# Kernel optimization log

Hardware: AMD Instinct MI355X
Metric: run time of the kernel (lower is better)

Reference implementation:

```python
import jax, jax.numpy as jnp
import numpy as np

N_NODES = 100000
N_EDGES = 1600000
NUM_FEATURES = 512
NHID = 256
CHEB_K = 6


def setup_inputs() -> dict:
    key = jax.random.key(0)
    ks = jax.random.split(key, 12)
    x = jax.random.normal(ks[0], (N_NODES, NUM_FEATURES), dtype=jnp.float32)
    edge_index = jax.random.randint(ks[1], (2, N_EDGES), 0, N_NODES, dtype=jnp.int64)
    edge_weight = jax.random.uniform(ks[2], (N_EDGES,), dtype=jnp.float32)
    s = 1.0 / np.sqrt(NUM_FEATURES)
    W1 = jax.random.uniform(ks[3], (NUM_FEATURES, NHID), jnp.float32, -s, s)
    b1 = jnp.zeros((NHID,), jnp.float32)
    s2 = 1.0 / np.sqrt(NHID)
    Wc = jax.random.uniform(ks[4], (CHEB_K, NHID, NHID // 2), jnp.float32, -s2, s2)
    bc = jnp.zeros((NHID // 2,), jnp.float32)
    s3 = 1.0 / np.sqrt(NHID // 2)
    W_out = jax.random.uniform(ks[5], (NHID // 2, 1), jnp.float32, -s3, s3)
    W_root = jax.random.uniform(ks[6], (NHID // 2, 1), jnp.float32, -s3, s3)
    b3 = jnp.zeros((1,), jnp.float32)
    return {"x": x, "edge_index": edge_index, "edge_weight": edge_weight,
            "W1": W1, "b1": b1, "Wc": Wc, "bc": bc,
            "W_out": W_out, "W_root": W_root, "b3": b3}


def _safe_rsqrt(d):
    return jnp.where(d > 0, jax.lax.rsqrt(jnp.where(d > 0, d, 1.0)), 0.0)


def _gcn_conv(x, src, dst, ew, W, b, n):
    # GCNConv: add self-loops (weight 1), sym-normalize, then aggregate x @ W.
    loop = jnp.arange(n)
    src2 = jnp.concatenate([src, loop])
    dst2 = jnp.concatenate([dst, loop])
    ew2 = jnp.concatenate([ew, jnp.ones((n,), ew.dtype)])
    deg = jax.ops.segment_sum(ew2, dst2, num_segments=n)
    dis = _safe_rsqrt(deg)
    norm = dis[src2] * ew2 * dis[dst2]                     # [E+N]
    h = x @ W                                              # [N, out]
    out = jax.ops.segment_sum(h[src2] * norm[:, None], dst2, num_segments=n)
    return out + b


def _cheb_conv(x, src, dst, ew, Wc, bc, n):
    # ChebConv (sym norm, lambda_max=2): L_hat = -D^{-1/2} A D^{-1/2} (diag 0).
    deg = jax.ops.segment_sum(ew, dst, num_segments=n)
    dis = _safe_rsqrt(deg)
    wn = -(dis[src] * ew * dis[dst])                        # [E]

    def lmv(h):  # L_hat @ h
        return jax.ops.segment_sum(h[src] * wn[:, None], dst, num_segments=n)

    Tx0 = x
    out = Tx0 @ Wc[0]
    Tx1 = lmv(x)
    out = out + Tx1 @ Wc[1]
    for k in range(2, Wc.shape[0]):
        Tx2 = 2.0 * lmv(Tx1) - Tx0
        out = out + Tx2 @ Wc[k]
        Tx0, Tx1 = Tx1, Tx2
    return out + bc


def _cluster_gcn_conv(x, src, dst, W_out, W_root, b, n):
    # ClusterGCNConv (diag_lambda=0): out = (D^{-1}(A+I) x) W_out + b + x W_root.
    loop = jnp.arange(n)
    src2 = jnp.concatenate([src, loop])
    dst2 = jnp.concatenate([dst, loop])
    deg = jax.ops.segment_sum(jnp.ones_like(dst2, dtype=x.dtype), dst2, num_segments=n)
    w = (1.0 / jnp.maximum(deg, 1.0))[dst2]                 # [E+N]
    agg = jax.ops.segment_sum(x[src2] * w[:, None], dst2, num_segments=n)
    return agg @ W_out + b + x @ W_root


def reference(x, edge_index, edge_weight, W1, b1, Wc, bc, W_out, W_root, b3):
    n = x.shape[0]
    src, dst = edge_index[0], edge_index[1]
    h = _gcn_conv(x, src, dst, edge_weight, W1, b1, n)
    h = jax.nn.relu(h)
    # dropout is identity in eval mode
    h = _cheb_conv(h, src, dst, edge_weight, Wc, bc, n)
    h = jax.nn.relu(h)
    features = h
    out = _cluster_gcn_conv(h, src, dst, W_out, W_root, b3, n)
    return (out.reshape(-1), features)
```

## Files before the change

kernel.cpp:

```cpp
#include <hip/hip_runtime.h>
#include <cstdint>
#include <cstddef>

typedef __attribute__((ext_vector_type(8))) short bf16x8;
typedef __attribute__((ext_vector_type(4))) float f32x4;

static inline int ceil_div(int a, int b){ return (a + b - 1) / b; }

struct HL { short h, l; };
__device__ inline HL split2(float a){
  unsigned u = __float_as_uint(a);
  unsigned hb = (u + 0x8000u) & 0xFFFF0000u;
  float r = a - __uint_as_float(hb);
  HL o;
  o.h = (short)(hb >> 16);
  o.l = (short)((__float_as_uint(r) + 0x8000u) >> 16);
  return o;
}

__device__ inline unsigned short f2b(float f){
  unsigned u = __float_as_uint(f);
  unsigned r = u + 0x7FFFu + ((u >> 16) & 1u);
  return (unsigned short)(r >> 16);
}
__device__ inline float b2f(unsigned short s){
  return __uint_as_float((unsigned)s << 16);
}

__global__ __launch_bounds__(256) void k_detect(const int* __restrict__ ei32, int E, int* __restrict__ flag){
  int t = blockIdx.x * 256 + threadIdx.x;
  if (t < 4096) {
    long long idx = 2LL * t + 1;
    if (idx < 2LL * E && ei32[idx] != 0) atomicOr(flag, 1);
  }
}

__global__ __launch_bounds__(256) void k_count(const void* __restrict__ ei, int E,
                                               const int* __restrict__ flag, int* __restrict__ cnt){
  int e = blockIdx.x * 256 + threadIdx.x;
  if (e >= E) return;
  int dst = (*flag) ? ((const int*)ei)[(size_t)E + e]
                    : (int)((const long long*)ei)[(size_t)E + e];
  atomicAdd(&cnt[dst], 1);
}

__global__ __launch_bounds__(256) void k_scan_part(const int* __restrict__ cnt, int* __restrict__ bsum, int N){
  int base = blockIdx.x * 1024 + threadIdx.x * 4;
  int s = 0;
  if (base + 4 <= N){
    int4 v = *(const int4*)(cnt + base);
    s = v.x + v.y + v.z + v.w;
  } else {
    for (int i = base; i < N; ++i) s += cnt[i];
  }
#pragma unroll
  for (int off = 32; off; off >>= 1) s += __shfl_xor(s, off);
  __shared__ int ws[4];
  if ((threadIdx.x & 63) == 0) ws[threadIdx.x >> 6] = s;
  __syncthreads();
  if (threadIdx.x == 0) bsum[blockIdx.x] = ws[0] + ws[1] + ws[2] + ws[3];
}

__global__ __launch_bounds__(1024) void k_scan_bsum(int* __restrict__ bsum, int nb){
  __shared__ int sh[1024];
  int t = threadIdx.x;
  int v = (t < nb) ? bsum[t] : 0;
  sh[t] = v; __syncthreads();
  for (int off = 1; off < 1024; off <<= 1){
    int u = (t >= off) ? sh[t - off] : 0;
    __syncthreads();
    sh[t] += u;
    __syncthreads();
  }
  if (t < nb) bsum[t] = sh[t] - v;
}

__global__ __launch_bounds__(256) void k_scan_write(const int* __restrict__ cnt, const int* __restrict__ bsum,
                                                    int* __restrict__ row_ptr, int* __restrict__ cursor,
                                                    int N, int E){
  int t = threadIdx.x;
  int base = blockIdx.x * 1024 + t * 4;
  int v0 = 0, v1 = 0, v2 = 0, v3 = 0;
  if (base + 4 <= N){
    int4 v = *(const int4*)(cnt + base);
    v0 = v.x; v1 = v.y; v2 = v.z; v3 = v.w;
  } else {
    if (base + 0 < N) v0 = cnt[base + 0];
    if (base + 1 < N) v1 = cnt[base + 1];
    if (base + 2 < N) v2 = cnt[base + 2];
    if (base + 3 < N) v3 = cnt[base + 3];
  }
  int s = v0 + v1 + v2 + v3;
  int lane = t & 63;
  int inc = s;
#pragma unroll
  for (int off = 1; off < 64; off <<= 1){
    int u = __shfl_up(inc, off);
    if (lane >= off) inc += u;
  }
  __shared__ int ws[4];
  if (lane == 63) ws[t >> 6] = inc;
  __syncthreads();
  int wid = t >> 6;
  int woff = 0;
  for (int i = 0; i < wid; ++i) woff += ws[i];
  int exc = bsum[blockIdx.x] + woff + inc - s;
  int p0 = exc, p1 = p0 + v0, p2 = p1 + v1, p3 = p2 + v2;
  if (base + 0 < N){ row_ptr[base + 0] = p0; cursor[base + 0] = p0; }
  if (base + 1 < N){ row_ptr[base + 1] = p1; cursor[base + 1] = p1; }
  if (base + 2 < N){ row_ptr[base + 2] = p2; cursor[base + 2] = p2; }
  if (base + 3 < N){ row_ptr[base + 3] = p3; cursor[base + 3] = p3; }
  if (blockIdx.x == 0 && t == 0) row_ptr[N] = E;
}

__global__ __launch_bounds__(256) void k_fill(const void* __restrict__ ei, const float* __restrict__ ew, int E,
                                              const int* __restrict__ flag, int* __restrict__ cursor,
                                              uint2* __restrict__ csr_sw){
  int e = blockIdx.x * 256 + threadIdx.x;
  if (e >= E) return;
  int src, dst;
  if (*flag){ src = ((const int*)ei)[e]; dst = ((const int*)ei)[(size_t)E + e]; }
  else      { src = (int)((const long long*)ei)[e]; dst = (int)((const long long*)ei)[(size_t)E + e]; }
  int pos = atomicAdd(&cursor[dst], 1);
  csr_sw[pos] = make_uint2((unsigned)src, __float_as_uint(ew[e]));
}

__global__ __launch_bounds__(256) void k_degrees(const int* __restrict__ row_ptr, const uint2* __restrict__ csr_sw,
                                                 float* __restrict__ dis1, float* __restrict__ dis2,
                                                 float* __restrict__ invw, int N){
  int r = blockIdx.x * 256 + threadIdx.x;
  if (r >= N) return;
  int e0 = row_ptr[r], e1 = row_ptr[r + 1];
  float s = 0.f;
  for (int e = e0; e < e1; ++e) s += __uint_as_float(csr_sw[e].y);
  dis1[r] = rsqrtf(s + 1.0f);
  dis2[r] = (s > 0.0f) ? rsqrtf(s) : 0.0f;
  invw[r] = 1.0f / (float)(e1 - e0 + 1);
}

__global__ __launch_bounds__(256) void k_norm(const uint2* __restrict__ csr_sw,
                                              const float* __restrict__ dis1, const float* __restrict__ dis2,
                                              uint2* __restrict__ pk_gcn, uint2* __restrict__ pk_cheb, int E){
  int e = blockIdx.x * 256 + threadIdx.x;
  if (e >= E) return;
  uint2 p = csr_sw[e];
  int s = (int)p.x;
  float w = __uint_as_float(p.y);
  pk_gcn[e]  = make_uint2(p.x, __float_as_uint(w * dis1[s]));
  pk_cheb[e] = make_uint2(p.x, __float_as_uint(w * dis2[s]));
}

__global__ __launch_bounds__(256) void k_prep_w(const float* __restrict__ W, short* __restrict__ Wh,
                                                short* __restrict__ Wl, int K, int N){
  int idx = blockIdx.x * 256 + threadIdx.x;
  if (idx >= K * N) return;
  int n = idx / K, k = idx - n * K;
  HL s = split2(W[(size_t)k * N + n]);
  Wh[idx] = s.h; Wl[idx] = s.l;
}

__global__ __launch_bounds__(256) void k_prep_wc(const float* __restrict__ Wc, short* __restrict__ Wh){
  int idx = blockIdx.x * 256 + threadIdx.x;
  if (idx >= 768 * 256) return;
  int n = idx >> 8, k = idx & 255;
  Wh[idx] = (short)f2b(Wc[(size_t)(n >> 7) * 256 * 128 + (size_t)k * 128 + (n & 127)]);
}

__global__ __launch_bounds__(256) void k_gemm_mfma(
    const float* __restrict__ A,
    const short* __restrict__ Bh, const short* __restrict__ Bl,
    unsigned short* __restrict__ Cb,
    int M, int Ncols, int K, int nbm)
{
  __shared__ short Ah[128][40];
  __shared__ short Bhs[128][40];
  __shared__ short Bls[128][40];
  int bid = blockIdx.x;
  int g = bid & 7, j = bid >> 3;
  int m_tile = g + 8 * (j >> 1);
  int n_tile = j & 1;
  if (m_tile >= nbm) return;
  int m0 = m_tile * 128, n0 = n_tile * 128;
  int t = threadIdx.x;
  int lane = t & 63, wid = t >> 6;
  int wr = wid >> 1, wc = wid & 1;
  int fr = lane & 15, fq = lane >> 4;
  int srow = t >> 1, skh = (t & 1) << 4;

  f32x4 acc[4][4];
#pragma unroll
  for (int i = 0; i < 4; ++i)
#pragma unroll
    for (int jj = 0; jj < 4; ++jj) acc[i][jj] = (f32x4){0.f, 0.f, 0.f, 0.f};

  bool aval = (m0 + srow) < M;
  const float* Aptr = A + (size_t)(m0 + srow) * K + skh;
  const short* Bhp = Bh + (size_t)(n0 + srow) * K + skh;
  const short* Blp = Bl + (size_t)(n0 + srow) * K + skh;

  float4 a0, a1, a2, a3;
  if (aval){
    const float4* ap = (const float4*)Aptr;
    a0 = ap[0]; a1 = ap[1]; a2 = ap[2]; a3 = ap[3];
  } else a0 = a1 = a2 = a3 = make_float4(0.f, 0.f, 0.f, 0.f);

  for (int k0 = 0; k0 < K; k0 += 32){
    bf16x8 h0, h1;
    h0[0]=(short)f2b(a0.x); h0[1]=(short)f2b(a0.y); h0[2]=(short)f2b(a0.z); h0[3]=(short)f2b(a0.w);
    h0[4]=(short)f2b(a1.x); h0[5]=(short)f2b(a1.y); h0[6]=(short)f2b(a1.z); h0[7]=(short)f2b(a1.w);
    h1[0]=(short)f2b(a2.x); h1[1]=(short)f2b(a2.y); h1[2]=(short)f2b(a2.z); h1[3]=(short)f2b(a2.w);
    h1[4]=(short)f2b(a3.x); h1[5]=(short)f2b(a3.y); h1[6]=(short)f2b(a3.z); h1[7]=(short)f2b(a3.w);
    *(bf16x8*)&Ah[srow][skh]     = h0;
    *(bf16x8*)&Ah[srow][skh + 8] = h1;
    {
      const bf16x8* bp = (const bf16x8*)(Bhp + k0);
      *(bf16x8*)&Bhs[srow][skh]     = bp[0];
      *(bf16x8*)&Bhs[srow][skh + 8] = bp[1];
      const bf16x8* cp = (const bf16x8*)(Blp + k0);
      *(bf16x8*)&Bls[srow][skh]     = cp[0];
      *(bf16x8*)&Bls[srow][skh + 8] = cp[1];
    }
    __syncthreads();
    bool more = (k0 + 32) < K;
    float4 n0v, n1v, n2v, n3v;
    if (more && aval){
      const float4* ap = (const float4*)(Aptr + k0 + 32);
      n0v = ap[0]; n1v = ap[1]; n2v = ap[2]; n3v = ap[3];
    } else n0v = n1v = n2v = n3v = make_float4(0.f, 0.f, 0.f, 0.f);
    bf16x8 afh[4], bfh[4], bfl[4];
#pragma unroll
    for (int m = 0; m < 4; ++m){
      int r = wr * 64 + m * 16 + fr;
      afh[m] = *(const bf16x8*)&Ah[r][fq * 8];
    }
#pragma unroll
    for (int n = 0; n < 4; ++n){
      int r = wc * 64 + n * 16 + fr;
      bfh[n] = *(const bf16x8*)&Bhs[r][fq * 8];
      bfl[n] = *(const bf16x8*)&Bls[r][fq * 8];
    }
#pragma unroll
    for (int m = 0; m < 4; ++m)
#pragma unroll
      for (int n = 0; n < 4; ++n){
        acc[m][n] = __builtin_amdgcn_mfma_f32_16x16x32_bf16(afh[m], bfh[n], acc[m][n], 0, 0, 0);
        acc[m][n] = __builtin_amdgcn_mfma_f32_16x16x32_bf16(afh[m], bfl[n], acc[m][n], 0, 0, 0);
      }
    __syncthreads();
    a0 = n0v; a1 = n1v; a2 = n2v; a3 = n3v;
  }
#pragma unroll
  for (int m = 0; m < 4; ++m){
#pragma unroll
    for (int n = 0; n < 4; ++n){
      int col = n0 + wc * 64 + n * 16 + fr;
#pragma unroll
      for (int r = 0; r < 4; ++r){
        int row = m0 + wr * 64 + m * 16 + fq * 4 + r;
        if (row < M){
          Cb[(size_t)row * Ncols + col] = f2b(acc[m][n][r]);
        }
      }
    }
  }
}

__global__ __launch_bounds__(256) void k_gemm_mfma2(
    const unsigned short* __restrict__ Ahg,
    const short* __restrict__ Bh,
    unsigned short* __restrict__ Cb, unsigned short* __restrict__ C5c,
    int M, int Ncols, int K, int nbm)
{
  __shared__ short Ah[128][40];
  __shared__ short Bhs[128][40];
  int bid = blockIdx.x;
  int g = bid & 7, j = bid >> 3;
  int m_tile = g + 8 * (j / 6);
  int n_tile = j - 6 * (j / 6);
  if (m_tile >= nbm) return;
  int m0 = m_tile * 128, n0 = n_tile * 128;
  int t = threadIdx.x;
  int lane = t & 63, wid = t >> 6;
  int wr = wid >> 1, wc = wid & 1;
  int fr = lane & 15, fq = lane >> 4;
  int srow = t >> 1, skh = (t & 1) << 4;

  f32x4 acc[4][4];
#pragma unroll
  for (int i = 0; i < 4; ++i)
#pragma unroll
    for (int jj = 0; jj < 4; ++jj) acc[i][jj] = (f32x4){0.f, 0.f, 0.f, 0.f};

  bool aval = (m0 + srow) < M;
  const unsigned short* Ahp = Ahg + (size_t)(m0 + srow) * K + skh;
  const short* Bhp = Bh + (size_t)(n0 + srow) * K + skh;

  bf16x8 ch0, ch1;
  if (aval){
    const bf16x8* ah = (const bf16x8*)Ahp;
    ch0 = ah[0]; ch1 = ah[1];
  } else {
    bf16x8 z = (bf16x8){0,0,0,0,0,0,0,0};
    ch0 = ch1 = z;
  }

  for (int k0 = 0; k0 < K; k0 += 32){
    *(bf16x8*)&Ah[srow][skh]     = ch0;
    *(bf16x8*)&Ah[srow][skh + 8] = ch1;
    {
      const bf16x8* bp = (const bf16x8*)(Bhp + k0);
      *(bf16x8*)&Bhs[srow][skh]     = bp[0];
      *(bf16x8*)&Bhs[srow][skh + 8] = bp[1];
    }
    __syncthreads();
    bool more = (k0 + 32) < K;
    bf16x8 nh0, nh1;
    if (more && aval){
      const bf16x8* ah = (const bf16x8*)(Ahp + k0 + 32);
      nh0 = ah[0]; nh1 = ah[1];
    } else {
      bf16x8 z = (bf16x8){0,0,0,0,0,0,0,0};
      nh0 = nh1 = z;
    }
    bf16x8 afh[4], bfh[4];
#pragma unroll
    for (int m = 0; m < 4; ++m){
      int r = wr * 64 + m * 16 + fr;
      afh[m] = *(const bf16x8*)&Ah[r][fq * 8];
    }
#pragma unroll
    for (int n = 0; n < 4; ++n){
      int r = wc * 64 + n * 16 + fr;
      bfh[n] = *(const bf16x8*)&Bhs[r][fq * 8];
    }
#pragma unroll
    for (int m = 0; m < 4; ++m)
#pragma unroll
      for (int n = 0; n < 4; ++n){
        acc[m][n] = __builtin_amdgcn_mfma_f32_16x16x32_bf16(afh[m], bfh[n], acc[m][n], 0, 0, 0);
      }
    __syncthreads();
    ch0 = nh0; ch1 = nh1;
  }
#pragma unroll
  for (int m = 0; m < 4; ++m){
#pragma unroll
    for (int n = 0; n < 4; ++n){
      int col = n0 + wc * 64 + n * 16 + fr;
#pragma unroll
      for (int r = 0; r < 4; ++r){
        int row = m0 + wr * 64 + m * 16 + fq * 4 + r;
        if (row < M){
          unsigned short v = f2b(acc[m][n][r]);
          Cb[(size_t)row * Ncols + col] = v;
          if (n_tile == 5) C5c[(size_t)row * 128 + (col - 640)] = v;
        }
      }
    }
  }
}

__global__ __launch_bounds__(256) void k_gcn_agg(
    const unsigned short* __restrict__ h0b,
    const uint2* __restrict__ pk, const int* __restrict__ row_ptr,
    const float* __restrict__ dis1, const float* __restrict__ b1,
    unsigned short* __restrict__ h1b, int N){
  int lane = threadIdx.x & 63;
  int r = blockIdx.x * 4 + (threadIdx.x >> 6);
  if (r >= N) return;
  float dr = dis1[r];
  ushort4 sv = ((const ushort4*)(h0b + (size_t)r * 256))[lane];
  float4 inner = make_float4(b2f(sv.x) * dr, b2f(sv.y) * dr, b2f(sv.z) * dr, b2f(sv.w) * dr);
  int e0 = row_ptr[r], e1 = row_ptr[r + 1];
  int e = e0;
  for (; e + 8 <= e1; e += 8){
    uint2 pv[8]; ushort4 vi[8];
#pragma unroll
    for (int q = 0; q < 8; ++q) pv[q] = pk[e + q];
#pragma unroll
    for (int q = 0; q < 8; ++q) vi[q] = ((const ushort4*)(h0b + (size_t)pv[q].x * 256))[lane];
#pragma unroll
    for (int q = 0; q < 8; ++q){
      float w = __uint_as_float(pv[q].y);
      inner.x = fmaf(w, b2f(vi[q].x), inner.x);
      inner.y = fmaf(w, b2f(vi[q].y), inner.y);
      inner.z = fmaf(w, b2f(vi[q].z), inner.z);
      inner.w = fmaf(w, b2f(vi[q].w), inner.w);
    }
  }
  for (; e < e1; ++e){
    uint2 p = pk[e];
    float w = __uint_as_float(p.y);
    ushort4 v = ((const ushort4*)(h0b + (size_t)p.x * 256))[lane];
    inner.x = fmaf(w, b2f(v.x), inner.x); inner.y = fmaf(w, b2f(v.y), inner.y);
    inner.z = fmaf(w, b2f(v.z), inner.z); inner.w = fmaf(w, b2f(v.w), inner.w);
  }
  float4 bb = ((const float4*)b1)[lane];
  ushort4 o;
  o.x = f2b(fmaxf(fmaf(inner.x, dr, bb.x), 0.f));
  o.y = f2b(fmaxf(fmaf(inner.y, dr, bb.y), 0.f));
  o.z = f2b(fmaxf(fmaf(inner.z, dr, bb.z), 0.f));
  o.w = f2b(fmaxf(fmaf(inner.w, dr, bb.w), 0.f));
  ((ushort4*)(h1b + (size_t)r * 256))[lane] = o;
}

__global__ __launch_bounds__(256) void k_cheb_spmm2(
    const unsigned short* __restrict__ Ck, int ckstride,
    const unsigned short* __restrict__ sub16, int substride,
    const float* __restrict__ subf,
    const unsigned short* __restrict__ srcb, int sstride,
    float* __restrict__ dst, unsigned short* __restrict__ dstb,
    const uint2* __restrict__ pk, const int* __restrict__ row_ptr,
    const float* __restrict__ dis2, float coef, int N){
  int lane = threadIdx.x & 63;
  int r = blockIdx.x * 4 + (threadIdx.x >> 6);
  if (r >= N) return;
  float2 inner = make_float2(0.f, 0.f);
  int e0 = row_ptr[r], e1 = row_ptr[r + 1];
  int e = e0;
  for (; e + 8 <= e1; e += 8){
    uint2 pv[8]; unsigned vi[8];
#pragma unroll
    for (int q = 0; q < 8; ++q) pv[q] = pk[e + q];
#pragma unroll
    for (int q = 0; q < 8; ++q) vi[q] = ((const unsigned*)(srcb + (size_t)pv[q].x * sstride))[lane];
#pragma unroll
    for (int q = 0; q < 8; ++q){
      float w = __uint_as_float(pv[q].y);
      inner.x = fmaf(w, __uint_as_float(vi[q] << 16), inner.x);
      inner.y = fmaf(w, __uint_as_float(vi[q] & 0xFFFF0000u), inner.y);
    }
  }
  for (; e < e1; ++e){
    uint2 p = pk[e];
    float w = __uint_as_float(p.y);
    unsigned v = ((const unsigned*)(srcb + (size_t)p.x * sstride))[lane];
    inner.x = fmaf(w, __uint_as_float(v << 16), inner.x);
    inner.y = fmaf(w, __uint_as_float(v & 0xFFFF0000u), inner.y);
  }
  float c = coef * dis2[r];
  unsigned ckv = ((const unsigned*)(Ck + (size_t)r * ckstride))[lane];
  float rx = fmaf(c, inner.x, __uint_as_float(ckv << 16));
  float ry = fmaf(c, inner.y, __uint_as_float(ckv & 0xFFFF0000u));
  if (sub16){
    unsigned sv = ((const unsigned*)(sub16 + (size_t)r * substride))[lane];
    rx -= __uint_as_float(sv << 16);
    ry -= __uint_as_float(sv & 0xFFFF0000u);
  }
  if (subf){
    float2 s2 = ((const float2*)(subf + (size_t)r * 128))[lane];
    rx -= s2.x;
    ry -= s2.y;
  }
  ((float2*)(dst + (size_t)r * 128))[lane] = make_float2(rx, ry);
  if (dstb){
    unsigned pkd = (unsigned)f2b(rx) | ((unsigned)f2b(ry) << 16);
    ((unsigned*)(dstb + (size_t)r * 128))[lane] = pkd;
  }
}

__global__ __launch_bounds__(256) void k_spmm_final(
    const unsigned short* __restrict__ Ck, int ckstride,
    const float* __restrict__ subf,
    const unsigned short* __restrict__ srcb, int sstride,
    const float* __restrict__ bc, const float* __restrict__ W_out, const float* __restrict__ W_root,
    float* __restrict__ feat, float* __restrict__ p, float* __restrict__ wr,
    const uint2* __restrict__ pk, const int* __restrict__ row_ptr,
    const float* __restrict__ dis2, float coef, int N){
  int lane = threadIdx.x & 63;
  int r = blockIdx.x * 4 + (threadIdx.x >> 6);
  if (r >= N) return;
  float2 inner = make_float2(0.f, 0.f);
  int e0 = row_ptr[r], e1 = row_ptr[r + 1];
  int e = e0;
  for (; e + 8 <= e1; e += 8){
    uint2 pv[8]; unsigned vi[8];
#pragma unroll
    for (int q = 0; q < 8; ++q) pv[q] = pk[e + q];
#pragma unroll
    for (int q = 0; q < 8; ++q) vi[q] = ((const unsigned*)(srcb + (size_t)pv[q].x * sstride))[lane];
#pragma unroll
    for (int q = 0; q < 8; ++q){
      float w = __uint_as_float(pv[q].y);
      inner.x = fmaf(w, __uint_as_float(vi[q] << 16), inner.x);
      inner.y = fmaf(w, __uint_as_float(vi[q] & 0xFFFF0000u), inner.y);
    }
  }
  for (; e < e1; ++e){
    uint2 pp = pk[e];
    float w = __uint_as_float(pp.y);
    unsigned v = ((const unsigned*)(srcb + (size_t)pp.x * sstride))[lane];
    inner.x = fmaf(w, __uint_as_float(v << 16), inner.x);
    inner.y = fmaf(w, __uint_as_float(v & 0xFFFF0000u), inner.y);
  }
  float c = coef * dis2[r];
  unsigned ckv = ((const unsigned*)(Ck + (size_t)r * ckstride))[lane];
  float rx = fmaf(c, inner.x, __uint_as_float(ckv << 16));
  float ry = fmaf(c, inner.y, __uint_as_float(ckv & 0xFFFF0000u));
  float2 s2 = ((const float2*)(subf + (size_t)r * 128))[lane];
  rx -= s2.x;
  ry -= s2.y;
  float2 bb = ((const float2*)bc)[lane];
  rx = fmaxf(rx + bb.x, 0.f);
  ry = fmaxf(ry + bb.y, 0.f);
  ((float2*)(feat + (size_t)r * 128))[lane] = make_float2(rx, ry);
  float2 wo = ((const float2*)W_out)[lane];
  float2 wrt = ((const float2*)W_root)[lane];
  float pp2 = rx * wo.x + ry * wo.y;
  float rr = rx * wrt.x + ry * wrt.y;
#pragma unroll
  for (int off = 32; off; off >>= 1){
    pp2 += __shfl_xor(pp2, off);
    rr += __shfl_xor(rr, off);
  }
  if (lane == 0){ p[r] = pp2; wr[r] = rr; }
}

__global__ __launch_bounds__(256) void k_out(const float* __restrict__ p, const float* __restrict__ wr,
    const float* __restrict__ invw, const uint2* __restrict__ pk, const int* __restrict__ row_ptr,
    const float* __restrict__ b3, float* __restrict__ out, int N){
  int r = blockIdx.x * 256 + threadIdx.x;
  if (r >= N) return;
  float s = p[r];
  int e0 = row_ptr[r], e1 = row_ptr[r + 1];
  int e = e0;
  float acc[8] = {0.f,0.f,0.f,0.f,0.f,0.f,0.f,0.f};
  for (; e + 8 <= e1; e += 8){
    int si[8];
#pragma unroll
    for (int q = 0; q < 8; ++q) si[q] = (int)pk[e + q].x;
#pragma unroll
    for (int q = 0; q < 8; ++q) acc[q] += p[si[q]];
  }
  for (; e < e1; ++e) acc[0] += p[(int)pk[e].x];
  s += ((acc[0]+acc[1])+(acc[2]+acc[3])) + ((acc[4]+acc[5])+(acc[6]+acc[7]));
  out[r] = invw[r] * s + wr[r] + b3[0];
}

extern "C" void kernel_launch(void* const* d_in, const int* in_sizes, int n_in,
                              void* d_out, int out_size, void* d_ws, size_t ws_size,
                              hipStream_t stream){
  const float* x      = (const float*)d_in[0];
  const void*  ei     = d_in[1];
  const float* ew     = (const float*)d_in[2];
  const float* W1     = (const float*)d_in[3];
  const float* b1     = (const float*)d_in[4];
  const float* Wc     = (const float*)d_in[5];
  const float* bc     = (const float*)d_in[6];
  const float* W_out  = (const float*)d_in[7];
  const float* W_root = (const float*)d_in[8];
  const float* b3     = (const float*)d_in[9];
  const int N = in_sizes[0] / 512;
  const int E = in_sizes[2];

  char* w = (char*)d_ws;
  auto alloc = [&](size_t bytes)->void*{ void* r = (void*)w; w += (bytes + 255) & ~(size_t)255; return r; };
  unsigned short* h1b = (unsigned short*)alloc((size_t)N * 256 * 2 * 2);
  float* B0 = (float*)h1b;
  float* B1 = B0 + (size_t)N * 128;
  float* B2 = (float*)alloc((size_t)N * 128 * 4);
  unsigned short* C5c = (unsigned short*)B2;
  unsigned short* CC  = (unsigned short*)alloc((size_t)N * 768 * 2);
  unsigned short* h0b = (unsigned short*)alloc((size_t)N * 256 * 2);
  unsigned short* Bb0 = h0b;
  unsigned short* Bb1 = h0b + (size_t)N * 128;
  uint2* csr_sw  = (uint2*)alloc((size_t)E * 8);
  uint2* pk_gcn  = (uint2*)alloc((size_t)E * 8);
  uint2* pk_cheb = (uint2*)alloc((size_t)E * 8);
  int*   row_ptr = (int*)  alloc((size_t)(N + 1) * 4);
  int*   cursor  = (int*)  alloc((size_t)N * 4);
  int*   cnt     = (int*)  alloc((size_t)N * 4);
  int*   bsum    = (int*)  alloc((size_t)1024 * 4);
  float* dis1    = (float*)alloc((size_t)N * 4);
  float* dis2    = (float*)alloc((size_t)N * 4);
  float* invw    = (float*)alloc((size_t)N * 4);
  float* pbuf    = (float*)alloc((size_t)N * 4);
  float* wrbuf   = (float*)alloc((size_t)N * 4);
  short* W1t_h   = (short*)alloc((size_t)512 * 256 * 2);
  short* W1t_l   = (short*)alloc((size_t)512 * 256 * 2);
  short* Wct_h   = (short*)alloc((size_t)768 * 256 * 2);
  int*   flag    = (int*)  alloc(256);

  hipMemsetAsync(cnt, 0, (size_t)N * 4, stream);
  hipMemsetAsync(flag, 0, 4, stream);

  k_detect<<<16, 256, 0, stream>>>((const int*)ei, E, flag);
  k_count<<<ceil_div(E, 256), 256, 0, stream>>>(ei, E, flag, cnt);
  int nb = ceil_div(N, 1024);
  k_scan_part<<<nb, 256, 0, stream>>>(cnt, bsum, N);
  k_scan_bsum<<<1, 1024, 0, stream>>>(bsum, nb);
  k_scan_write<<<nb, 256, 0, stream>>>(cnt, bsum, row_ptr, cursor, N, E);
  k_fill<<<ceil_div(E, 256), 256, 0, stream>>>(ei, ew, E, flag, cursor, csr_sw);
  k_degrees<<<ceil_div(N, 256), 256, 0, stream>>>(row_ptr, csr_sw, dis1, dis2, invw, N);
  k_norm<<<ceil_div(E, 256), 256, 0, stream>>>(csr_sw, dis1, dis2, pk_gcn, pk_cheb, E);

  k_prep_w<<<ceil_div(512 * 256, 256), 256, 0, stream>>>(W1, W1t_h, W1t_l, 512, 256);
  k_prep_wc<<<ceil_div(768 * 256, 256), 256, 0, stream>>>(Wc, Wct_h);

  int nbm = ceil_div(N, 128);
  int grid1 = 8 * 2 * ceil_div(nbm, 8);
  k_gemm_mfma<<<grid1, 256, 0, stream>>>(x, W1t_h, W1t_l, h0b, N, 256, 512, nbm);
  k_gcn_agg<<<ceil_div(N, 4), 256, 0, stream>>>(h0b, pk_gcn, row_ptr, dis1, b1, h1b, N);

  int grid2 = 8 * 6 * ceil_div(nbm, 8);
  k_gemm_mfma2<<<grid2, 256, 0, stream>>>(h1b, Wct_h, CC, C5c, N, 768, 256, nbm);

  auto spmm = [&](const unsigned short* Ck, const unsigned short* s16, int s16s, const float* sf,
                  const unsigned short* src, int ss, float* dst, unsigned short* dstb, float coef){
    k_cheb_spmm2<<<ceil_div(N, 4), 256, 0, stream>>>(Ck, 768, s16, s16s, sf, src, ss, dst, dstb,
        pk_cheb, row_ptr, dis2, coef, N);
  };
  spmm(CC + 4*128, nullptr, 0, nullptr, C5c, 128, B0, Bb0, -2.f);
  spmm(CC + 3*128, C5c, 128, nullptr, Bb0, 128, B1, Bb1, -2.f);
  spmm(CC + 2*128, nullptr, 0, B0, Bb1, 128, B2, Bb0, -2.f);
  spmm(CC + 1*128, nullptr, 0, B1, Bb0, 128, B0, Bb1, -2.f);

  float* out  = (float*)d_out;
  float* feat = out + N;
  k_spmm_final<<<ceil_div(N, 4), 256, 0, stream>>>(CC + 0*128, 768, B2, Bb1, 128,
      bc, W_out, W_root, feat, pbuf, wrbuf, pk_cheb, row_ptr, dis2, -1.f, N);
  k_out<<<ceil_div(N, 256), 256, 0, stream>>>(pbuf, wrbuf, invw, pk_cheb, row_ptr, b3, out, N);
}
```

Measured before the change: 1.037 ms.

## Build CSR via two-level bucket partition with shared-memory atomics

```diff
diff --git a/kernel.cpp b/kernel.cpp
--- a/kernel.cpp
+++ b/kernel.cpp
@@ -27,6 +27,8 @@
   return __uint_as_float((unsigned)s << 16);
 }
 
+#define EPB 4096
+
 __global__ __launch_bounds__(256) void k_detect(const int* __restrict__ ei32, int E, int* __restrict__ flag){
   int t = blockIdx.x * 256 + threadIdx.x;
   if (t < 4096) {
@@ -35,107 +37,135 @@
   }
 }
 
-__global__ __launch_bounds__(256) void k_count(const void* __restrict__ ei, int E,
-                                               const int* __restrict__ flag, int* __restrict__ cnt){
-  int e = blockIdx.x * 256 + threadIdx.x;
-  if (e >= E) return;
-  int dst = (*flag) ? ((const int*)ei)[(size_t)E + e]
-                    : (int)((const long long*)ei)[(size_t)E + e];
-  atomicAdd(&cnt[dst], 1);
-}
-
-__global__ __launch_bounds__(256) void k_scan_part(const int* __restrict__ cnt, int* __restrict__ bsum, int N){
-  int base = blockIdx.x * 1024 + threadIdx.x * 4;
-  int s = 0;
-  if (base + 4 <= N){
-    int4 v = *(const int4*)(cnt + base);
-    s = v.x + v.y + v.z + v.w;
-  } else {
-    for (int i = base; i < N; ++i) s += cnt[i];
-  }
-#pragma unroll
-  for (int off = 32; off; off >>= 1) s += __shfl_xor(s, off);
-  __shared__ int ws[4];
-  if ((threadIdx.x & 63) == 0) ws[threadIdx.x >> 6] = s;
+__global__ __launch_bounds__(256) void k_hist(const void* __restrict__ ei, int E,
+                                              const int* __restrict__ flag, int* __restrict__ block_hist){
+  __shared__ int h[512];
+  for (int i = threadIdx.x; i < 512; i += 256) h[i] = 0;
   __syncthreads();
-  if (threadIdx.x == 0) bsum[blockIdx.x] = ws[0] + ws[1] + ws[2] + ws[3];
-}
-
-__global__ __launch_bounds__(1024) void k_scan_bsum(int* __restrict__ bsum, int nb){
-  __shared__ int sh[1024];
+  int base = blockIdx.x * EPB;
+  bool is32 = (*flag != 0);
+  for (int i = 0; i < 16; ++i){
+    int e = base + i * 256 + threadIdx.x;
+    if (e < E){
+      int dst = is32 ? ((const int*)ei)[(size_t)E + e] : (int)((const long long*)ei)[(size_t)E + e];
+      atomicAdd(&h[dst >> 8], 1);
+    }
+  }
+  __syncthreads();
+  for (int i = threadIdx.x; i < 512; i += 256) block_hist[blockIdx.x * 512 + i] = h[i];
+}
+
+__global__ __launch_bounds__(64) void k_colscan(const int* __restrict__ block_hist, int* __restrict__ off_hist,
+                                                int* __restrict__ bucket_total, int nblk){
+  int k = blockIdx.x;
+  int lane = threadIdx.x;
+  int carry = 0;
+  for (int c = 0; c * 64 < nblk; ++c){
+    int b = c * 64 + lane;
+    int v = (b < nblk) ? block_hist[b * 512 + k] : 0;
+    int inc = v;
+#pragma unroll
+    for (int off = 1; off < 64; off <<= 1){
+      int u = __shfl_up(inc, off);
+      if (lane >= off) inc += u;
+    }
+    if (b < nblk) off_hist[b * 512 + k] = carry + inc - v;
+    carry += __shfl(inc, 63);
+  }
+  if (lane == 0) bucket_total[k] = carry;
+}
+
+__global__ __launch_bounds__(512) void k_bucketbase(const int* __restrict__ bucket_total,
+                                                    int* __restrict__ bucket_base,
+                                                    int* __restrict__ row_ptr, int N, int E){
+  __shared__ int sh[512];
   int t = threadIdx.x;
-  int v = (t < nb) ? bsum[t] : 0;
+  int v = bucket_total[t];
   sh[t] = v; __syncthreads();
-  for (int off = 1; off < 1024; off <<= 1){
+  for (int off = 1; off < 512; off <<= 1){
     int u = (t >= off) ? sh[t - off] : 0;
     __syncthreads();
     sh[t] += u;
     __syncthreads();
   }
-  if (t < nb) bsum[t] = sh[t] - v;
-}
-
-__global__ __launch_bounds__(256) void k_scan_write(const int* __restrict__ cnt, const int* __restrict__ bsum,
-                                                    int* __restrict__ row_ptr, int* __restrict__ cursor,
-                                                    int N, int E){
+  bucket_base[t] = sh[t] - v;
+  if (t == 511) bucket_base[512] = sh[511];
+  if (t == 0) row_ptr[N] = E;
+}
+
+__global__ __launch_bounds__(256) void k_partition(const void* __restrict__ ei, const float* __restrict__ ew,
+                                                   int E, const int* __restrict__ flag,
+                                                   const int* __restrict__ off_hist,
+                                                   const int* __restrict__ bucket_base,
+                                                   uint2* __restrict__ part){
+  __shared__ int cur[512];
+  for (int i = threadIdx.x; i < 512; i += 256)
+    cur[i] = off_hist[blockIdx.x * 512 + i] + bucket_base[i];
+  __syncthreads();
+  int base = blockIdx.x * EPB;
+  bool is32 = (*flag != 0);
+  for (int i = 0; i < 16; ++i){
+    int e = base + i * 256 + threadIdx.x;
+    if (e < E){
+      int src, dst;
+      if (is32){ src = ((const int*)ei)[e]; dst = ((const int*)ei)[(size_t)E + e]; }
+      else     { src = (int)((const long long*)ei)[e]; dst = (int)((const long long*)ei)[(size_t)E + e]; }
+      int pos = atomicAdd(&cur[dst >> 8], 1);
+      part[pos] = make_uint2((unsigned)src | ((unsigned)(dst & 255) << 20), __float_as_uint(ew[e]));
+    }
+  }
+}
+
+__global__ __launch_bounds__(256) void k_bucket_csr(const uint2* __restrict__ part,
+                                                    const int* __restrict__ bucket_base,
+                                                    uint2* __restrict__ csr_sw, int* __restrict__ row_ptr,
+                                                    float* __restrict__ dis1, float* __restrict__ dis2,
+                                                    float* __restrict__ invw, int N){
+  __shared__ int cnt[256];
+  __shared__ float wsum[256];
+  __shared__ int cursor[256];
+  __shared__ int ws[4];
+  int k = blockIdx.x;
   int t = threadIdx.x;
-  int base = blockIdx.x * 1024 + t * 4;
-  int v0 = 0, v1 = 0, v2 = 0, v3 = 0;
-  if (base + 4 <= N){
-    int4 v = *(const int4*)(cnt + base);
-    v0 = v.x; v1 = v.y; v2 = v.z; v3 = v.w;
-  } else {
-    if (base + 0 < N) v0 = cnt[base + 0];
-    if (base + 1 < N) v1 = cnt[base + 1];
-    if (base + 2 < N) v2 = cnt[base + 2];
-    if (base + 3 < N) v3 = cnt[base + 3];
-  }
-  int s = v0 + v1 + v2 + v3;
+  int base = bucket_base[k], end = bucket_base[k + 1];
+  cnt[t] = 0; wsum[t] = 0.f;
+  __syncthreads();
+  for (int i = base + t; i < end; i += 256){
+    uint2 rec = part[i];
+    int dstl = (rec.x >> 20) & 255;
+    atomicAdd(&cnt[dstl], 1);
+    atomicAdd(&wsum[dstl], __uint_as_float(rec.y));
+  }
+  __syncthreads();
+  int v = cnt[t];
   int lane = t & 63;
-  int inc = s;
+  int inc = v;
 #pragma unroll
   for (int off = 1; off < 64; off <<= 1){
     int u = __shfl_up(inc, off);
     if (lane >= off) inc += u;
   }
-  __shared__ int ws[4];
   if (lane == 63) ws[t >> 6] = inc;
   __syncthreads();
-  int wid = t >> 6;
   int woff = 0;
-  for (int i = 0; i < wid; ++i) woff += ws[i];
-  int exc = bsum[blockIdx.x] + woff + inc - s;
-  int p0 = exc, p1 = p0 + v0, p2 = p1 + v1, p3 = p2 + v2;
-  if (base + 0 < N){ row_ptr[base + 0] = p0; cursor[base + 0] = p0; }
-  if (base + 1 < N){ row_ptr[base + 1] = p1; cursor[base + 1] = p1; }
-  if (base + 2 < N){ row_ptr[base + 2] = p2; cursor[base + 2] = p2; }
-  if (base + 3 < N){ row_ptr[base + 3] = p3; cursor[base + 3] = p3; }
-  if (blockIdx.x == 0 && t == 0) row_ptr[N] = E;
-}
-
-__global__ __launch_bounds__(256) void k_fill(const void* __restrict__ ei, const float* __restrict__ ew, int E,
-                                              const int* __restrict__ flag, int* __restrict__ cursor,
-                                              uint2* __restrict__ csr_sw){
-  int e = blockIdx.x * 256 + threadIdx.x;
-  if (e >= E) return;
-  int src, dst;
-  if (*flag){ src = ((const int*)ei)[e]; dst = ((const int*)ei)[(size_t)E + e]; }
-  else      { src = (int)((const long long*)ei)[e]; dst = (int)((const long long*)ei)[(size_t)E + e]; }
-  int pos = atomicAdd(&cursor[dst], 1);
-  csr_sw[pos] = make_uint2((unsigned)src, __float_as_uint(ew[e]));
-}
-
-__global__ __launch_bounds__(256) void k_degrees(const int* __restrict__ row_ptr, const uint2* __restrict__ csr_sw,
-                                                 float* __restrict__ dis1, float* __restrict__ dis2,
-                                                 float* __restrict__ invw, int N){
-  int r = blockIdx.x * 256 + threadIdx.x;
-  if (r >= N) return;
-  int e0 = row_ptr[r], e1 = row_ptr[r + 1];
-  float s = 0.f;
-  for (int e = e0; e < e1; ++e) s += __uint_as_float(csr_sw[e].y);
-  dis1[r] = rsqrtf(s + 1.0f);
-  dis2[r] = (s > 0.0f) ? rsqrtf(s) : 0.0f;
-  invw[r] = 1.0f / (float)(e1 - e0 + 1);
+  for (int i = 0; i < (t >> 6); ++i) woff += ws[i];
+  int exc = woff + inc - v;
+  int node = k * 256 + t;
+  if (node < N){
+    row_ptr[node] = base + exc;
+    float s = wsum[t];
+    dis1[node] = rsqrtf(s + 1.0f);
+    dis2[node] = (s > 0.f) ? rsqrtf(s) : 0.f;
+    invw[node] = 1.0f / (float)(v + 1);
+  }
+  cursor[t] = exc;
+  __syncthreads();
+  for (int i = base + t; i < end; i += 256){
+    uint2 rec = part[i];
+    int dstl = (rec.x >> 20) & 255;
+    int pos = base + atomicAdd(&cursor[dstl], 1);
+    csr_sw[pos] = make_uint2(rec.x & 0xFFFFFu, rec.y);
+  }
 }
 
 __global__ __launch_bounds__(256) void k_norm(const uint2* __restrict__ csr_sw,
@@ -567,10 +597,13 @@
   uint2* csr_sw  = (uint2*)alloc((size_t)E * 8);
   uint2* pk_gcn  = (uint2*)alloc((size_t)E * 8);
   uint2* pk_cheb = (uint2*)alloc((size_t)E * 8);
+  uint2* part    = (uint2*)alloc((size_t)E * 8);
+  int nblk = ceil_div(E, EPB);
+  int*   block_hist  = (int*)alloc((size_t)nblk * 512 * 4);
+  int*   off_hist    = (int*)alloc((size_t)nblk * 512 * 4);
+  int*   bucket_total= (int*)alloc(512 * 4);
+  int*   bucket_base = (int*)alloc(513 * 4);
   int*   row_ptr = (int*)  alloc((size_t)(N + 1) * 4);
-  int*   cursor  = (int*)  alloc((size_t)N * 4);
-  int*   cnt     = (int*)  alloc((size_t)N * 4);
-  int*   bsum    = (int*)  alloc((size_t)1024 * 4);
   float* dis1    = (float*)alloc((size_t)N * 4);
   float* dis2    = (float*)alloc((size_t)N * 4);
   float* invw    = (float*)alloc((size_t)N * 4);
@@ -581,17 +614,15 @@
   short* Wct_h   = (short*)alloc((size_t)768 * 256 * 2);
   int*   flag    = (int*)  alloc(256);
 
-  hipMemsetAsync(cnt, 0, (size_t)N * 4, stream);
   hipMemsetAsync(flag, 0, 4, stream);
 
   k_detect<<<16, 256, 0, stream>>>((const int*)ei, E, flag);
-  k_count<<<ceil_div(E, 256), 256, 0, stream>>>(ei, E, flag, cnt);
-  int nb = ceil_div(N, 1024);
-  k_scan_part<<<nb, 256, 0, stream>>>(cnt, bsum, N);
-  k_scan_bsum<<<1, 1024, 0, stream>>>(bsum, nb);
-  k_scan_write<<<nb, 256, 0, stream>>>(cnt, bsum, row_ptr, cursor, N, E);
-  k_fill<<<ceil_div(E, 256), 256, 0, stream>>>(ei, ew, E, flag, cursor, csr_sw);
-  k_degrees<<<ceil_div(N, 256), 256, 0, stream>>>(row_ptr, csr_sw, dis1, dis2, invw, N);
+  k_hist<<<nblk, 256, 0, stream>>>(ei, E, flag, block_hist);
+  k_colscan<<<512, 64, 0, stream>>>(block_hist, off_hist, bucket_total, nblk);
+  k_bucketbase<<<1, 512, 0, stream>>>(bucket_total, bucket_base, row_ptr, N, E);
+  k_partition<<<nblk, 256, 0, stream>>>(ei, ew, E, flag, off_hist, bucket_base, part);
+  int nbkt = ceil_div(N, 256);
+  k_bucket_csr<<<nbkt, 256, 0, stream>>>(part, bucket_base, csr_sw, row_ptr, dis1, dis2, invw, N);
   k_norm<<<ceil_div(E, 256), 256, 0, stream>>>(csr_sw, dis1, dis2, pk_gcn, pk_cheb, E);
 
   k_prep_w<<<ceil_div(512 * 256, 256), 256, 0, stream>>>(W1, W1t_h, W1t_l, 512, 256);
```

After: 907.0 us. -12.5%, faster.
